# Optimization experiments

Measured on AMD Instinct MI355X. Metric: run time of the kernel, lower is better.

## Reference

```python
import jax, jax.numpy as jnp
import numpy as np

N, D = 32, 2                 # nodes, dof per node (dof_ndim)
BS = 4096
ZD = 2 * N * D               # state dim = 128
EDGE_I = np.arange(N - 1)    # chain edges (i, i+1)
EDGE_J = np.arange(1, N)
C = N                        # 1 tether + (N-1) distance constraints


def _minv(p, m_params):
    # point-mass (d2ids key 0) block mass-matrix inverse: diagonal per node
    inv_m = jnp.exp(-m_params[:, 0])            # (N,)
    return p * inv_m[:, None]


def _potential(r_flat, W0, b0, W1, b1, W2, b2, W3, b3):
    # V_net: mlp([N*D, h, h, h, 1], Softplus) followed by Reshape(-1)
    h = jax.nn.softplus(r_flat @ W0 + b0)
    h = jax.nn.softplus(h @ W1 + b1)
    h = jax.nn.softplus(h @ W2 + b2)
    return (h @ W3 + b3)[..., 0]                # (bs,)


def _hamiltonian(z, m_params, W0, b0, W1, b1, W2, b2, W3, b3):
    bs = z.shape[0]
    r = z[:, : ZD // 2].reshape(bs, N, D)
    p = z[:, ZD // 2 :].reshape(bs, N, D)
    T = 0.5 * jnp.sum(p * _minv(p, m_params), axis=(-1, -2))   # EuclideanT
    V = _potential(r.reshape(bs, -1), W0, b0, W1, b1, W2, b2, W3, b3)
    return T + V


def _rigid_dphi(r, v):
    # DPhi of shape (bs, 2, N, D, 2, C); axis1 = d/d(r,v), axis4 = (phi, phidot)
    # constraint 0: tether |r_0|^2 - l^2; constraints 1..N-1: |r_i - r_j|^2 - l^2
    bs = r.shape[0]
    dphi_dr = jnp.zeros((bs, N, D, C), r.dtype)
    dphidot_dr = jnp.zeros((bs, N, D, C), r.dtype)
    dphi_dr = dphi_dr.at[:, 0, :, 0].set(2.0 * r[:, 0])
    dphidot_dr = dphidot_dr.at[:, 0, :, 0].set(2.0 * v[:, 0])
    dr = 2.0 * (r[:, EDGE_I] - r[:, EDGE_J])    # (bs, N-1, D)
    dv = 2.0 * (v[:, EDGE_I] - v[:, EDGE_J])
    cidx = np.arange(1, N)
    dr_t = jnp.swapaxes(dr, 0, 1)               # (N-1, bs, D) for fancy-index scatter
    dv_t = jnp.swapaxes(dv, 0, 1)
    dphi_dr = dphi_dr.at[:, EDGE_I, :, cidx].add(dr_t)
    dphi_dr = dphi_dr.at[:, EDGE_J, :, cidx].add(-dr_t)
    dphidot_dr = dphidot_dr.at[:, EDGE_I, :, cidx].add(dv_t)
    dphidot_dr = dphidot_dr.at[:, EDGE_J, :, cidx].add(-dv_t)
    zeros = jnp.zeros_like(dphi_dr)
    d_r = jnp.stack([dphi_dr, dphidot_dr], axis=-2)   # (bs, N, D, 2, C)
    d_v = jnp.stack([zeros, dphi_dr], axis=-2)        # dphi/dv=0, dphidot/dv=dphi/dr
    return jnp.stack([d_r, d_v], axis=1)              # (bs, 2, N, D, 2, C)


def _chnn_dphi(z, m_params):
    bs = z.shape[0]
    zr = z.reshape(bs, 2, N, D)
    r, p = zr[:, 0], zr[:, 1]
    r_dot = _minv(p, m_params)
    DPhi = _rigid_dphi(r, r_dot)
    # convert velocity derivative to momentum derivative via Minv
    dv = _minv(DPhi[:, 1].reshape(bs, N, -1), m_params).reshape(DPhi[:, 1].shape)
    DPhi = jnp.stack([DPhi[:, 0], dv], axis=1)
    return DPhi.reshape(bs, 2 * N * D, -1)            # (bs, ZD, 2C)


def _J(M):
    # canonical symplectic map applied to column(s): J [a; b] = [b; -a]
    Dm = M.shape[-2]
    return jnp.concatenate([M[..., Dm // 2 :, :], -M[..., : Dm // 2, :]], axis=-2)


def setup_inputs() -> dict:
    key = jax.random.key(0)
    ks = jax.random.split(key, 8)
    return {
        "t": jnp.zeros((1,), jnp.float32),
        "z": jax.random.normal(ks[0], (BS, ZD), jnp.float32),
        "m_params": 0.1 * jax.random.normal(ks[1], (N, 1), jnp.float32),
        "W0": 0.1 * jax.random.normal(ks[2], (N * D, 256), jnp.float32),
        "b0": jnp.zeros((256,), jnp.float32),
        "W1": 0.1 * jax.random.normal(ks[3], (256, 256), jnp.float32),
        "b1": jnp.zeros((256,), jnp.float32),
        "W2": 0.1 * jax.random.normal(ks[4], (256, 256), jnp.float32),
        "b2": jnp.zeros((256,), jnp.float32),
        "W3": 0.1 * jax.random.normal(ks[5], (256, 1), jnp.float32),
        "b3": jnp.zeros((1,), jnp.float32),
    }


def reference(t, z, m_params, W0, b0, W1, b1, W2, b2, W3, b3):
    # constrained Hamiltonian vector field: P(J dH), P = I - J DPhi (DPhi^T J DPhi)^{-1} DPhi^T
    grad_H = jax.grad(
        lambda zz: _hamiltonian(zz, m_params, W0, b0, W1, b1, W2, b2, W3, b3).sum()
    )
    dH = grad_H(z)                          # (bs, ZD)
    DPhi = _chnn_dphi(z, m_params)          # (bs, ZD, 2C)
    JdH = _J(dH[..., None])                 # (bs, ZD, 1)
    DPhiT = jnp.swapaxes(DPhi, -1, -2)      # (bs, 2C, ZD)
    A = DPhiT @ _J(DPhi)                    # (bs, 2C, 2C)
    X = jnp.linalg.solve(A, DPhiT @ JdH)    # (bs, 2C, 1)
    return (JdH - _J(DPhi @ X))[..., 0]     # (bs, ZD)
```

## Files before the change

kernel.cpp:

```cpp
#include <hip/hip_runtime.h>

#define ZD   128
#define NP   32
#define SPB  16
#define NBLK (4096 / SPB)
#define NTH  512

typedef __attribute__((ext_vector_type(8))) short bf16x8;
typedef __attribute__((ext_vector_type(4))) float f32x4;

#define OFF_W0   0
#define OFF_W1   16384
#define OFF_W2   81920
#define OFF_W2T  147456
#define OFF_W1T  212992
#define OFF_W0T  278528

__device__ __forceinline__ float softplus_f(float x) {
    float e = __expf(-fabsf(x));
    return fmaxf(x, 0.0f) + __logf(1.0f + e);
}
__device__ __forceinline__ float sigmoid_f(float x) {
    return 1.0f / (1.0f + __expf(-x));
}
__device__ __forceinline__ unsigned short f2b(float f) {
    unsigned int u = __float_as_uint(f);
    unsigned int r = (u + 0x7FFFu + ((u >> 16) & 1u)) >> 16;
    return (unsigned short)r;
}

__global__ void prep_pack(const float* __restrict__ W0,
                          const float* __restrict__ W1,
                          const float* __restrict__ W2,
                          short* __restrict__ P) {
    int T = blockIdx.x * 256 + threadIdx.x;
    if (T >= 36864) return;
    const float* src; int base, NT, trans, lu, t = T;
    if (t < 2048)               { src = W0; base = OFF_W0;  NT = 16; trans = 0; lu = t; }
    else if ((t -= 2048) < 8192){ src = W1; base = OFF_W1;  NT = 16; trans = 0; lu = t; }
    else if ((t -= 8192) < 8192){ src = W2; base = OFF_W2;  NT = 16; trans = 0; lu = t; }
    else if ((t -= 8192) < 8192){ src = W2; base = OFF_W2T; NT = 16; trans = 1; lu = t; }
    else if ((t -= 8192) < 8192){ src = W1; base = OFF_W1T; NT = 16; trans = 1; lu = t; }
    else              { t -= 8192; src = W0; base = OFF_W0T; NT = 4; trans = 1; lu = t; }
    int frag = lu >> 6, lane = lu & 63;
    int kb = frag / NT, nt = frag - kb * NT;
    int n  = nt * 16 + (lane & 15);
    int k0 = kb * 32 + ((lane >> 4) << 3);
    int N  = NT * 16;
    bf16x8 hv;
    #pragma unroll
    for (int j = 0; j < 8; ++j) {
        int k = k0 + j;
        float w = trans ? src[n * 256 + k] : src[k * N + n];
        hv[j] = (short)f2b(w);
    }
    ((bf16x8*)(P + base))[lu] = hv;
}

template<int KB, int NT, int TPW>
__device__ __forceinline__ void load_B(const short* __restrict__ BH,
                                       int L, int wvx, bf16x8* dst) {
    #pragma unroll
    for (int kb = 0; kb < KB; ++kb)
        #pragma unroll
        for (int t = 0; t < TPW; ++t)
            dst[kb * TPW + t] = ((const bf16x8*)BH)[(kb * NT + wvx * TPW + t) * 64 + L];
}

template<int KB, int TPW>
__device__ __forceinline__ void mfma_B(const unsigned short (*aH)[264],
                                       int L, int quad,
                                       const bf16x8* fr, f32x4* acc) {
    #pragma unroll
    for (int kb = 0; kb < KB; ++kb) {
        bf16x8 ah = *(const bf16x8*)&aH[L & 15][kb * 32 + quad * 8];
        #pragma unroll
        for (int t = 0; t < TPW; ++t)
            acc[t] = __builtin_amdgcn_mfma_f32_16x16x32_bf16(ah, fr[kb * TPW + t],
                                                             acc[t], 0, 0, 0);
    }
}

__global__ __launch_bounds__(NTH, 2) void chnn_main(
    const float* __restrict__ z, const float* __restrict__ mp,
    const float* __restrict__ B0, const float* __restrict__ B1,
    const float* __restrict__ B2, const float* __restrict__ W3,
    const short* __restrict__ P,
    float* __restrict__ out)
{
    __shared__ __align__(16) unsigned short actH[2][16][264];
    __shared__ __align__(16) float rsh[64][SPB];
    __shared__ __align__(16) float vsh[64][SPB];
    __shared__ __align__(16) float gsh[64][SPB];
    __shared__ float invm[NP];
    __shared__ double invmd[NP];
    __shared__ float ge[SPB][NP][2], gd[SPB][NP][2];
    __shared__ double Sdd[SPB][NP], Sed[SPB][NP], Ked[SPB][NP];
    __shared__ double b0d[SPB][NP], b1d[SPB][NP];
    __shared__ double wfac[SPB][NP], dinv[SPB][NP];

    const int tid  = threadIdx.x;
    const int L    = tid & 63;
    const int wv   = tid >> 6;
    const int quad = L >> 4;
    const long sbase = (long)blockIdx.x * SPB;

    if (tid < NP) {
        double e = exp(-(double)mp[tid]);
        invmd[tid] = e;
        invm[tid] = (float)e;
    }

    bf16x8 frA[16], frB[16];
    load_B<2, 16, 2>(P + OFF_W0, L, wv, frA);

    const float* zb = z + sbase * ZD;
    #pragma unroll
    for (int k = 0; k < 4; ++k) {
        int e = k * NTH + tid;
        int s = e >> 7, idx = e & 127;
        float val = zb[e];
        if (idx < 64) {
            rsh[idx][s] = val;
            actH[0][s][idx] = f2b(val);
        } else {
            vsh[idx - 64][s] = val;
        }
    }
    __syncthreads();
    {
        float* pv = &vsh[0][0];
        #pragma unroll
        for (int k = 0; k < 2; ++k) {
            int e = k * NTH + tid;
            pv[e] *= invm[e >> 5];
        }
    }
    __syncthreads();

    f32x4 acc[2];
    float p0s[2][4], p1s[2][4];
    const int nbase = wv * 32 + (L & 15);

    load_B<8, 16, 2>(P + OFF_W1, L, wv, frB);
    #pragma unroll
    for (int t = 0; t < 2; ++t) {
        float bb = B0[nbase + t * 16];
        acc[t] = (f32x4){bb, bb, bb, bb};
    }
    mfma_B<2, 2>(actH[0], L, quad, frA, acc);
    #pragma unroll
    for (int t = 0; t < 2; ++t) {
        int n = nbase + t * 16;
        #pragma unroll
        for (int r = 0; r < 4; ++r) {
            p0s[t][r] = acc[t][r];
            actH[1][quad * 4 + r][n] = f2b(softplus_f(acc[t][r]));
        }
    }
    __syncthreads();

    load_B<8, 16, 2>(P + OFF_W2, L, wv, frA);
    #pragma unroll
    for (int t = 0; t < 2; ++t) {
        float bb = B1[nbase + t * 16];
        acc[t] = (f32x4){bb, bb, bb, bb};
    }
    mfma_B<8, 2>(actH[1], L, quad, frB, acc);
    #pragma unroll
    for (int t = 0; t < 2; ++t) {
        int n = nbase + t * 16;
        #pragma unroll
        for (int r = 0; r < 4; ++r) {
            p1s[t][r] = acc[t][r];
            actH[0][quad * 4 + r][n] = f2b(softplus_f(acc[t][r]));
        }
    }
    __syncthreads();

    load_B<8, 16, 2>(P + OFF_W2T, L, wv, frB);
    #pragma unroll
    for (int t = 0; t < 2; ++t) {
        float bb = B2[nbase + t * 16];
        acc[t] = (f32x4){bb, bb, bb, bb};
    }
    mfma_B<8, 2>(actH[0], L, quad, frA, acc);
    #pragma unroll
    for (int t = 0; t < 2; ++t) {
        int n = nbase + t * 16;
        float w3 = W3[n];
        #pragma unroll
        for (int r = 0; r < 4; ++r)
            actH[1][quad * 4 + r][n] = f2b(w3 * sigmoid_f(acc[t][r]));
    }
    __syncthreads();

    load_B<8, 16, 2>(P + OFF_W1T, L, wv, frA);
    #pragma unroll
    for (int t = 0; t < 2; ++t) acc[t] = (f32x4){0.f, 0.f, 0.f, 0.f};
    mfma_B<8, 2>(actH[1], L, quad, frB, acc);
    #pragma unroll
    for (int t = 0; t < 2; ++t) {
        int n = nbase + t * 16;
        #pragma unroll
        for (int r = 0; r < 4; ++r)
            actH[0][quad * 4 + r][n] = f2b(acc[t][r] * sigmoid_f(p1s[t][r]));
    }
    __syncthreads();

    if (wv < 4) load_B<8, 4, 1>(P + OFF_W0T, L, wv, frB);
    #pragma unroll
    for (int t = 0; t < 2; ++t) acc[t] = (f32x4){0.f, 0.f, 0.f, 0.f};
    mfma_B<8, 2>(actH[0], L, quad, frA, acc);
    #pragma unroll
    for (int t = 0; t < 2; ++t) {
        int n = nbase + t * 16;
        #pragma unroll
        for (int r = 0; r < 4; ++r)
            actH[1][quad * 4 + r][n] = f2b(acc[t][r] * sigmoid_f(p0s[t][r]));
    }
    __syncthreads();

    if (wv < 4) {
        acc[0] = (f32x4){0.f, 0.f, 0.f, 0.f};
        mfma_B<8, 1>(actH[1], L, quad, frB, acc);
        int i = wv * 16 + (L & 15);
        #pragma unroll
        for (int r = 0; r < 4; ++r)
            gsh[i][quad * 4 + r] = acc[0][r];
    }
    __syncthreads();

    {
        const int c = tid & 31;
        const int s = tid >> 5;
        double gx, gy, gdx, gdy;
        if (c == 0) {
            double r0x = rsh[0][s], r0y = rsh[1][s];
            double v0x = vsh[0][s], v0y = vsh[1][s];
            gx = 2.0 * r0x; gy = 2.0 * r0y; gdx = 2.0 * v0x; gdy = 2.0 * v0y;
            Sdd[s][0] = invmd[0] * (gx * gx + gy * gy);
            b0d[s][0] = gx * v0x + gy * v0y;
            b1d[s][0] = gdx * v0x + gdy * v0y
                      - invmd[0] * (gx * (double)gsh[0][s] + gy * (double)gsh[1][s]);
        } else {
            int aa = 2 * (c - 1), b = 2 * c;
            double dvx = (double)vsh[aa][s] - (double)vsh[b][s];
            double dvy = (double)vsh[aa + 1][s] - (double)vsh[b + 1][s];
            gx = 2.0 * ((double)rsh[aa][s] - (double)rsh[b][s]);
            gy = 2.0 * ((double)rsh[aa + 1][s] - (double)rsh[b + 1][s]);
            gdx = 2.0 * dvx; gdy = 2.0 * dvy;
            Sdd[s][c] = (invmd[c - 1] + invmd[c]) * (gx * gx + gy * gy);
            b0d[s][c] = gx * dvx + gy * dvy;
            double mgx = invmd[c - 1] * (double)gsh[aa][s]     - invmd[c] * (double)gsh[b][s];
            double mgy = invmd[c - 1] * (double)gsh[aa + 1][s] - invmd[c] * (double)gsh[b + 1][s];
            b1d[s][c] = gdx * dvx + gdy * dvy - (gx * mgx + gy * mgy);
        }
        ge[s][c][0] = (float)gx;  ge[s][c][1] = (float)gy;
        gd[s][c][0] = (float)gdx; gd[s][c][1] = (float)gdy;
        __syncthreads();
        if (c < 31) {
            double g1x = ge[s][c + 1][0], g1y = ge[s][c + 1][1];
            double q1x = gd[s][c + 1][0], q1y = gd[s][c + 1][1];
            if (c == 0) {
                Sed[s][0] = invmd[0] * (gx * g1x + gy * g1y);
                Ked[s][0] = invmd[0] * ((gdx * g1x + gdy * g1y) - (gx * q1x + gy * q1y));
            } else {
                Sed[s][c] = -invmd[c] * (gx * g1x + gy * g1y);
                Ked[s][c] =  invmd[c] * ((gx * q1x + gy * q1y) - (gdx * g1x + gdy * g1y));
            }
        }
    }
    __syncthreads();

    if (tid < SPB) {
        int s = tid;
        double d = Sdd[s][0];
        if (d == 0.0) d = 1e-300;
        dinv[s][0] = 1.0 / d;
        double y = b0d[s][0];
        for (int c = 1; c < NP; ++c) {
            double e = Sed[s][c - 1];
            double w = e * dinv[s][c - 1];
            wfac[s][c - 1] = w;
            d = Sdd[s][c] - w * e;
            if (d == 0.0) d = 1e-300;
            dinv[s][c] = 1.0 / d;
            y = b0d[s][c] - w * y;
            b0d[s][c] = y;
        }
        double x = b0d[s][31] * dinv[s][31];
        b0d[s][31] = x;
        for (int c = 30; c >= 0; --c) {
            x = (b0d[s][c] - Sed[s][c] * x) * dinv[s][c];
            b0d[s][c] = x;
        }
    }
    __syncthreads();

    {
        int c = tid & 31, s = tid >> 5;
        double kx = 0.0;
        if (c < 31) kx += Ked[s][c] * b0d[s][c + 1];
        if (c > 0)  kx -= Ked[s][c - 1] * b0d[s][c - 1];
        b1d[s][c] = kx - b1d[s][c];
    }
    __syncthreads();

    if (tid < SPB) {
        int s = tid;
        double y = b1d[s][0];
        for (int c = 1; c < NP; ++c) {
            y = b1d[s][c] - wfac[s][c - 1] * y;
            b1d[s][c] = y;
        }
        double x = b1d[s][31] * dinv[s][31];
        b1d[s][31] = x;
        for (int c = 30; c >= 0; --c) {
            x = (b1d[s][c] - Sed[s][c] * x) * dinv[s][c];
            b1d[s][c] = x;
        }
    }
    __syncthreads();

    float* ob = out + sbase * ZD;
    #pragma unroll
    for (int k = 0; k < 4; ++k) {
        int e = k * NTH + tid;
        int s = e >> 7, idx = e & 127;
        int j = idx & 63;
        int n = j >> 1, d = j & 1;
        float res;
        if (idx < 64) {
            double Gx1 = (n == 0) ? (double)ge[s][0][d] * b0d[s][0]
                                  : -(double)ge[s][n][d] * b0d[s][n];
            if (n < 31) Gx1 += (double)ge[s][n + 1][d] * b0d[s][n + 1];
            res = (float)((double)vsh[j][s] - invmd[n] * Gx1);
        } else {
            double Gx0 = (n == 0) ? (double)ge[s][0][d] * b1d[s][0]
                                  : -(double)ge[s][n][d] * b1d[s][n];
            if (n < 31) Gx0 += (double)ge[s][n + 1][d] * b1d[s][n + 1];
            double Gd1 = (n == 0) ? (double)gd[s][0][d] * b0d[s][0]
                                  : -(double)gd[s][n][d] * b0d[s][n];
            if (n < 31) Gd1 += (double)gd[s][n + 1][d] * b0d[s][n + 1];
            res = (float)(-(double)gsh[j][s] + Gx0 + Gd1);
        }
        ob[e] = res;
    }
}

extern "C" void kernel_launch(void* const* d_in, const int* in_sizes, int n_in,
                              void* d_out, int out_size, void* d_ws, size_t ws_size,
                              hipStream_t stream) {
    const float* z  = (const float*)d_in[1];
    const float* mp = (const float*)d_in[2];
    const float* W0 = (const float*)d_in[3];
    const float* B0 = (const float*)d_in[4];
    const float* W1 = (const float*)d_in[5];
    const float* B1 = (const float*)d_in[6];
    const float* W2 = (const float*)d_in[7];
    const float* B2 = (const float*)d_in[8];
    const float* W3 = (const float*)d_in[9];

    short* P = (short*)d_ws;

    prep_pack<<<144, 256, 0, stream>>>(W0, W1, W2, P);
    chnn_main<<<NBLK, NTH, 0, stream>>>(z, mp, B0, B1, B2, W3, P, (float*)d_out);
}
```

Baseline: 94.52 us.

## Double block size to 1024 threads with one MFMA tile per wave

Raises the block to 1024 threads (16 waves) so each wave computes a single 16-column MFMA tile instead of two, halving per-wave weight-fragment registers. Load/store loops and the tail phases are adjusted, and the upper 512 threads idle during the double-precision constraint stages, taking a matching extra barrier. The launch bound drops the 2-blocks hint. This trades more waves and finer parallelism in the MLP for more idle threads in the serial solve section and barriers across a larger block.

```diff
diff --git a/kernel.cpp b/kernel.cpp
--- a/kernel.cpp
+++ b/kernel.cpp
@@ -4,7 +4,7 @@
 #define NP   32
 #define SPB  16
 #define NBLK (4096 / SPB)
-#define NTH  512
+#define NTH  1024
 
 typedef __attribute__((ext_vector_type(8))) short bf16x8;
 typedef __attribute__((ext_vector_type(4))) float f32x4;
@@ -57,31 +57,26 @@
     ((bf16x8*)(P + base))[lu] = hv;
 }
 
-template<int KB, int NT, int TPW>
+template<int KB, int NT>
 __device__ __forceinline__ void load_B(const short* __restrict__ BH,
-                                       int L, int wvx, bf16x8* dst) {
+                                       int L, int tile, bf16x8* dst) {
     #pragma unroll
     for (int kb = 0; kb < KB; ++kb)
-        #pragma unroll
-        for (int t = 0; t < TPW; ++t)
-            dst[kb * TPW + t] = ((const bf16x8*)BH)[(kb * NT + wvx * TPW + t) * 64 + L];
-}
-
-template<int KB, int TPW>
+        dst[kb] = ((const bf16x8*)BH)[(kb * NT + tile) * 64 + L];
+}
+
+template<int KB>
 __device__ __forceinline__ void mfma_B(const unsigned short (*aH)[264],
                                        int L, int quad,
-                                       const bf16x8* fr, f32x4* acc) {
+                                       const bf16x8* fr, f32x4& acc) {
     #pragma unroll
     for (int kb = 0; kb < KB; ++kb) {
         bf16x8 ah = *(const bf16x8*)&aH[L & 15][kb * 32 + quad * 8];
-        #pragma unroll
-        for (int t = 0; t < TPW; ++t)
-            acc[t] = __builtin_amdgcn_mfma_f32_16x16x32_bf16(ah, fr[kb * TPW + t],
-                                                             acc[t], 0, 0, 0);
-    }
-}
-
-__global__ __launch_bounds__(NTH, 2) void chnn_main(
+        acc = __builtin_amdgcn_mfma_f32_16x16x32_bf16(ah, fr[kb], acc, 0, 0, 0);
+    }
+}
+
+__global__ __launch_bounds__(NTH) void chnn_main(
     const float* __restrict__ z, const float* __restrict__ mp,
     const float* __restrict__ B0, const float* __restrict__ B1,
     const float* __restrict__ B2, const float* __restrict__ W3,
@@ -111,12 +106,12 @@
         invm[tid] = (float)e;
     }
 
-    bf16x8 frA[16], frB[16];
-    load_B<2, 16, 2>(P + OFF_W0, L, wv, frA);
+    bf16x8 frA[8], frB[8];
+    load_B<2, 16>(P + OFF_W0, L, wv, frA);
 
     const float* zb = z + sbase * ZD;
     #pragma unroll
-    for (int k = 0; k < 4; ++k) {
+    for (int k = 0; k < 2; ++k) {
         int e = k * NTH + tid;
         int s = e >> 7, idx = e & 127;
         float val = zb[e];
@@ -130,108 +125,81 @@
     __syncthreads();
     {
         float* pv = &vsh[0][0];
-        #pragma unroll
-        for (int k = 0; k < 2; ++k) {
-            int e = k * NTH + tid;
-            pv[e] *= invm[e >> 5];
-        }
-    }
-    __syncthreads();
-
-    f32x4 acc[2];
-    float p0s[2][4], p1s[2][4];
-    const int nbase = wv * 32 + (L & 15);
-
-    load_B<8, 16, 2>(P + OFF_W1, L, wv, frB);
-    #pragma unroll
-    for (int t = 0; t < 2; ++t) {
-        float bb = B0[nbase + t * 16];
-        acc[t] = (f32x4){bb, bb, bb, bb};
-    }
-    mfma_B<2, 2>(actH[0], L, quad, frA, acc);
-    #pragma unroll
-    for (int t = 0; t < 2; ++t) {
-        int n = nbase + t * 16;
-        #pragma unroll
-        for (int r = 0; r < 4; ++r) {
-            p0s[t][r] = acc[t][r];
-            actH[1][quad * 4 + r][n] = f2b(softplus_f(acc[t][r]));
-        }
-    }
-    __syncthreads();
-
-    load_B<8, 16, 2>(P + OFF_W2, L, wv, frA);
-    #pragma unroll
-    for (int t = 0; t < 2; ++t) {
-        float bb = B1[nbase + t * 16];
-        acc[t] = (f32x4){bb, bb, bb, bb};
-    }
-    mfma_B<8, 2>(actH[1], L, quad, frB, acc);
-    #pragma unroll
-    for (int t = 0; t < 2; ++t) {
-        int n = nbase + t * 16;
-        #pragma unroll
-        for (int r = 0; r < 4; ++r) {
-            p1s[t][r] = acc[t][r];
-            actH[0][quad * 4 + r][n] = f2b(softplus_f(acc[t][r]));
-        }
-    }
-    __syncthreads();
-
-    load_B<8, 16, 2>(P + OFF_W2T, L, wv, frB);
-    #pragma unroll
-    for (int t = 0; t < 2; ++t) {
-        float bb = B2[nbase + t * 16];
-        acc[t] = (f32x4){bb, bb, bb, bb};
-    }
-    mfma_B<8, 2>(actH[0], L, quad, frA, acc);
-    #pragma unroll
-    for (int t = 0; t < 2; ++t) {
-        int n = nbase + t * 16;
-        float w3 = W3[n];
+        pv[tid] *= invm[tid >> 5];
+    }
+    __syncthreads();
+
+    f32x4 acc;
+    float p0s[4], p1s[4];
+    const int nbase = wv * 16 + (L & 15);
+
+    load_B<8, 16>(P + OFF_W1, L, wv, frB);
+    {
+        float bb = B0[nbase];
+        acc = (f32x4){bb, bb, bb, bb};
+    }
+    mfma_B<2>(actH[0], L, quad, frA, acc);
+    #pragma unroll
+    for (int r = 0; r < 4; ++r) {
+        p0s[r] = acc[r];
+        actH[1][quad * 4 + r][nbase] = f2b(softplus_f(acc[r]));
+    }
+    __syncthreads();
+
+    load_B<8, 16>(P + OFF_W2, L, wv, frA);
+    {
+        float bb = B1[nbase];
+        acc = (f32x4){bb, bb, bb, bb};
+    }
+    mfma_B<8>(actH[1], L, quad, frB, acc);
+    #pragma unroll
+    for (int r = 0; r < 4; ++r) {
+        p1s[r] = acc[r];
+        actH[0][quad * 4 + r][nbase] = f2b(softplus_f(acc[r]));
+    }
+    __syncthreads();
+
+    load_B<8, 16>(P + OFF_W2T, L, wv, frB);
+    {
+        float bb = B2[nbase];
+        acc = (f32x4){bb, bb, bb, bb};
+    }
+    mfma_B<8>(actH[0], L, quad, frA, acc);
+    {
+        float w3 = W3[nbase];
         #pragma unroll
         for (int r = 0; r < 4; ++r)
-            actH[1][quad * 4 + r][n] = f2b(w3 * sigmoid_f(acc[t][r]));
-    }
-    __syncthreads();
-
-    load_B<8, 16, 2>(P + OFF_W1T, L, wv, frA);
-    #pragma unroll
-    for (int t = 0; t < 2; ++t) acc[t] = (f32x4){0.f, 0.f, 0.f, 0.f};
-    mfma_B<8, 2>(actH[1], L, quad, frB, acc);
-    #pragma unroll
-    for (int t = 0; t < 2; ++t) {
-        int n = nbase + t * 16;
-        #pragma unroll
-        for (int r = 0; r < 4; ++r)
-            actH[0][quad * 4 + r][n] = f2b(acc[t][r] * sigmoid_f(p1s[t][r]));
-    }
-    __syncthreads();
-
-    if (wv < 4) load_B<8, 4, 1>(P + OFF_W0T, L, wv, frB);
-    #pragma unroll
-    for (int t = 0; t < 2; ++t) acc[t] = (f32x4){0.f, 0.f, 0.f, 0.f};
-    mfma_B<8, 2>(actH[0], L, quad, frA, acc);
-    #pragma unroll
-    for (int t = 0; t < 2; ++t) {
-        int n = nbase + t * 16;
-        #pragma unroll
-        for (int r = 0; r < 4; ++r)
-            actH[1][quad * 4 + r][n] = f2b(acc[t][r] * sigmoid_f(p0s[t][r]));
-    }
+            actH[1][quad * 4 + r][nbase] = f2b(w3 * sigmoid_f(acc[r]));
+    }
+    __syncthreads();
+
+    load_B<8, 16>(P + OFF_W1T, L, wv, frA);
+    acc = (f32x4){0.f, 0.f, 0.f, 0.f};
+    mfma_B<8>(actH[1], L, quad, frB, acc);
+    #pragma unroll
+    for (int r = 0; r < 4; ++r)
+        actH[0][quad * 4 + r][nbase] = f2b(acc[r] * sigmoid_f(p1s[r]));
+    __syncthreads();
+
+    if (wv < 4) load_B<8, 4>(P + OFF_W0T, L, wv, frB);
+    acc = (f32x4){0.f, 0.f, 0.f, 0.f};
+    mfma_B<8>(actH[0], L, quad, frA, acc);
+    #pragma unroll
+    for (int r = 0; r < 4; ++r)
+        actH[1][quad * 4 + r][nbase] = f2b(acc[r] * sigmoid_f(p0s[r]));
     __syncthreads();
 
     if (wv < 4) {
-        acc[0] = (f32x4){0.f, 0.f, 0.f, 0.f};
-        mfma_B<8, 1>(actH[1], L, quad, frB, acc);
+        acc = (f32x4){0.f, 0.f, 0.f, 0.f};
+        mfma_B<8>(actH[1], L, quad, frB, acc);
         int i = wv * 16 + (L & 15);
         #pragma unroll
         for (int r = 0; r < 4; ++r)
-            gsh[i][quad * 4 + r] = acc[0][r];
-    }
-    __syncthreads();
-
-    {
+            gsh[i][quad * 4 + r] = acc[r];
+    }
+    __syncthreads();
+
+    if (tid < 512) {
         const int c = tid & 31;
         const int s = tid >> 5;
         double gx, gy, gdx, gdy;
@@ -270,6 +238,8 @@
                 Ked[s][c] =  invmd[c] * ((gx * q1x + gy * q1y) - (gdx * g1x + gdy * g1y));
             }
         }
+    } else {
+        __syncthreads();
     }
     __syncthreads();
 
@@ -298,7 +268,7 @@
     }
     __syncthreads();
 
-    {
+    if (tid < 512) {
         int c = tid & 31, s = tid >> 5;
         double kx = 0.0;
         if (c < 31) kx += Ked[s][c] * b0d[s][c + 1];
@@ -325,7 +295,7 @@
 
     float* ob = out + sbase * ZD;
     #pragma unroll
-    for (int k = 0; k < 4; ++k) {
+    for (int k = 0; k < 2; ++k) {
         int e = k * NTH + tid;
         int s = e >> 7, idx = e & 127;
         int j = idx & 63;
```

After: 95.13 us. About the same (+0.6%).
